# Kernel optimization log

Measured on AMD Instinct MI355X. Metric: run time of the kernel, lower is better.

Reference implementation:

```python
import jax, jax.numpy as jnp
import numpy as np

TOTAL_LABELS = 21
TOTAL_POS = 128
TOTAL_NEG = 128
VARIANCES = jnp.asarray([0.1, 0.1, 0.2, 0.2], dtype=jnp.float32)


def _make_boxes(key, shape):
    # valid [y1,x1,y2,x2] boxes with y2>y1, x2>x1 in [0,1]
    k1, k2 = jax.random.split(key)
    lo = jax.random.uniform(k1, shape + (2,), dtype=jnp.float32) * 0.6
    sz = jax.random.uniform(k2, shape + (2,), dtype=jnp.float32) * 0.4 + 1e-3
    return jnp.concatenate([lo, lo + sz], axis=-1)


def setup_inputs() -> dict:
    key = jax.random.key(0)
    kr, kg, kl, kp, kn = jax.random.split(key, 5)
    B, N, M = 64, 3000, 128
    roi_bboxes = _make_boxes(kr, (B, N))
    gt_boxes = _make_boxes(kg, (B, M))
    gt_labels = jax.random.randint(kl, (B, M), 1, TOTAL_LABELS).astype(jnp.int32)
    maxval = max(TOTAL_POS, TOTAL_NEG) * 10  # matches tf.random.uniform(minval=1, maxval=10*count)
    rand_pos = jax.random.randint(kp, (B, N), 1, maxval).astype(jnp.int32)
    rand_neg = jax.random.randint(kn, (B, N), 1, maxval).astype(jnp.int32)
    return {"roi_bboxes": roi_bboxes, "gt_boxes": gt_boxes, "gt_labels": gt_labels,
            "rand_pos": rand_pos, "rand_neg": rand_neg}


def _iou_map(roi, gt):
    # roi: [B,N,4], gt: [B,M,4] -> iou: [B,N,M]
    r = roi[:, :, None, :]
    g = gt[:, None, :, :]
    iy1 = jnp.maximum(r[..., 0], g[..., 0])
    ix1 = jnp.maximum(r[..., 1], g[..., 1])
    iy2 = jnp.minimum(r[..., 2], g[..., 2])
    ix2 = jnp.minimum(r[..., 3], g[..., 3])
    inter = jnp.maximum(iy2 - iy1, 0.0) * jnp.maximum(ix2 - ix1, 0.0)
    area_r = (r[..., 2] - r[..., 0]) * (r[..., 3] - r[..., 1])
    area_g = (g[..., 2] - g[..., 0]) * (g[..., 3] - g[..., 1])
    return inter / (area_r + area_g - inter + 1e-7)


def _random_select(mask, rand_ints, count):
    # faithful port of train_utils.randomly_select_xyz_mask: rank by mask*rand, keep top `count`
    mult = mask.astype(jnp.int32) * rand_ints
    order = jnp.argsort(-mult, axis=-1)
    ranks = jnp.argsort(order, axis=-1)
    return mask & (ranks < count)


def _get_deltas(bboxes, gt):
    bw = bboxes[..., 3] - bboxes[..., 1]
    bh = bboxes[..., 2] - bboxes[..., 0]
    bcx = bboxes[..., 1] + 0.5 * bw
    bcy = bboxes[..., 0] + 0.5 * bh
    gw = gt[..., 3] - gt[..., 1]
    gh = gt[..., 2] - gt[..., 0]
    gcx = gt[..., 1] + 0.5 * gw
    gcy = gt[..., 0] + 0.5 * gh
    bw = jnp.where(bw == 0.0, 1e-3, bw)
    bh = jnp.where(bh == 0.0, 1e-3, bh)
    dx = jnp.where(gw == 0.0, 0.0, (gcx - bcx) / bw)
    dy = jnp.where(gh == 0.0, 0.0, (gcy - bcy) / bh)
    dw = jnp.where(gw == 0.0, 0.0, jnp.log(jnp.where(gw == 0.0, 1.0, gw / bw)))
    dh = jnp.where(gh == 0.0, 0.0, jnp.log(jnp.where(gh == 0.0, 1.0, gh / bh)))
    return jnp.stack([dy, dx, dh, dw], axis=-1)


def reference(roi_bboxes, gt_boxes, gt_labels, rand_pos, rand_neg):
    B, N = roi_bboxes.shape[:2]
    iou = _iou_map(roi_bboxes, gt_boxes)                      # [B,N,M]
    best_gt = jnp.argmax(iou, axis=2)                         # [B,N]
    best_iou = jnp.max(iou, axis=2)                           # [B,N]
    pos_mask = _random_select(best_iou > 0.5, rand_pos, TOTAL_POS)
    neg_mask = _random_select((best_iou < 0.5) & (best_iou > 0.1), rand_neg, TOTAL_NEG)
    gt_boxes_map = jnp.take_along_axis(gt_boxes, best_gt[:, :, None], axis=1)   # [B,N,4]
    expanded_gt_boxes = jnp.where(pos_mask[..., None], gt_boxes_map, 0.0)
    gt_labels_map = jnp.take_along_axis(gt_labels, best_gt, axis=1)             # [B,N]
    pos_gt_labels = jnp.where(pos_mask, gt_labels_map, -1)
    expanded_gt_labels = pos_gt_labels + neg_mask.astype(jnp.int32)
    deltas = _get_deltas(roi_bboxes, expanded_gt_boxes) / VARIANCES             # [B,N,4]
    roi_bbox_labels = jax.nn.one_hot(expanded_gt_labels, TOTAL_LABELS, dtype=deltas.dtype)  # [B,N,L]
    # broadcast-multiply scatter: place deltas into the slot of the assigned label
    roi_bbox_deltas = roi_bbox_labels[..., None] * deltas[:, :, None, :]        # [B,N,L,4]
    roi_bbox_deltas = roi_bbox_deltas.reshape(B, N * TOTAL_LABELS, 4)
    return (jax.lax.stop_gradient(roi_bbox_deltas), jax.lax.stop_gradient(roi_bbox_labels))
```

## Files before the change

### kernel.cpp

```cpp
#include <hip/hip_runtime.h>

#define BB 64
#define NN 3000
#define MM 128
#define NBINS 1280
#define NSEL 128

__global__ __launch_bounds__(256) void k1_iou(
    const float4* __restrict__ roi, const float4* __restrict__ gt,
    const int* __restrict__ gtl, const int* __restrict__ rpos,
    const int* __restrict__ rneg, int* __restrict__ packed,
    float4* __restrict__ deltas, float4* __restrict__ out1z)
{
  #pragma clang fp contract(off)
  const int b = blockIdx.y;
  const int n = blockIdx.x * 256 + threadIdx.x;
  const bool valid = (n < NN);
  __shared__ float4 g[MM];
  __shared__ float  ga[MM];
  __shared__ int    gl[MM];

  float4 r = roi[b * NN + (valid ? n : 0)];
  if (threadIdx.x < MM) {
    float4 v = gt[b * MM + threadIdx.x];
    g[threadIdx.x]  = v;
    ga[threadIdx.x] = (v.z - v.x) * (v.w - v.y);
    gl[threadIdx.x] = gtl[b * MM + threadIdx.x];
  }
  __syncthreads();

  {
    const float4 z = make_float4(0.f, 0.f, 0.f, 0.f);
    const int gid = (blockIdx.y * gridDim.x + blockIdx.x) * 256 + threadIdx.x;
    for (int i = gid; i < BB * NN * 21; i += 768 * 256) out1z[i] = z;
  }

  if (!valid) return;
  float ar = (r.z - r.x) * (r.w - r.y);
  float best = -1.0f; int bi = 0;
  #pragma unroll 4
  for (int m = 0; m < MM; ++m) {
    float4 gm = g[m];
    float iy1 = fmaxf(r.x, gm.x);
    float ix1 = fmaxf(r.y, gm.y);
    float iy2 = fminf(r.z, gm.z);
    float ix2 = fminf(r.w, gm.w);
    float inter = fmaxf(iy2 - iy1, 0.0f) * fmaxf(ix2 - ix1, 0.0f);
    float iou = inter / (ar + ga[m] - inter + 1e-7f);
    if (iou > best) { best = iou; bi = m; }
  }
  int pm = (best > 0.5f) ? rpos[b * NN + n] : 0;
  int nm = (best < 0.5f && best > 0.1f) ? rneg[b * NN + n] : 0;
  packed[b * NN + n] = pm | (nm << 11) | (gl[bi] << 22);

  float4 gg = g[bi];
  float bw = r.w - r.y, bh = r.z - r.x;
  float bcx = r.y + 0.5f * bw, bcy = r.x + 0.5f * bh;
  float gw = gg.w - gg.y, gh = gg.z - gg.x;
  float gcx = gg.y + 0.5f * gw, gcy = gg.x + 0.5f * gh;
  bw = (bw == 0.0f) ? 0.001f : bw;
  bh = (bh == 0.0f) ? 0.001f : bh;
  float dx = (gw == 0.0f) ? 0.0f : (gcx - bcx) / bw;
  float dy = (gh == 0.0f) ? 0.0f : (gcy - bcy) / bh;
  float dw = (gw == 0.0f) ? 0.0f : logf(gw / bw);
  float dh = (gh == 0.0f) ? 0.0f : logf(gh / bh);
  deltas[b * NN + n] = make_float4(dy / 0.1f, dx / 0.1f, dh / 0.2f, dw / 0.2f);
}

__global__ __launch_bounds__(1024) void k2_select(
    const int* __restrict__ packed, const float4* __restrict__ deltas,
    float4* __restrict__ out1, float* __restrict__ out2)
{
  const int b = blockIdx.x;
  const int tid = threadIdx.x;
  const int lane = tid & 63;
  const int wave = tid >> 6;
  __shared__ int sp[NN];
  __shared__ unsigned hist[NBINS + 1];
  __shared__ unsigned wsum[16];
  __shared__ int sT[4];

  for (int i = tid; i < NBINS + 1; i += 1024) hist[i] = 0;
  if (tid == 0) { sT[0] = 0; sT[1] = 0; sT[2] = 0; sT[3] = 0; }
  __syncthreads();

  for (int i = tid; i < NN; i += 1024) {
    int p = packed[b * NN + i];
    sp[i] = p;
    int pm = p & 0x7FF, nm = (p >> 11) & 0x7FF;
    if (pm) atomicAdd(&hist[pm], 1u);
    if (nm) atomicAdd(&hist[nm], 0x10000u);
  }
  __syncthreads();

  if (wave == 0) {
    unsigned cs[21];
    const int base = 1 + lane * 20;
    cs[20] = 0;
    #pragma unroll
    for (int j = 19; j >= 0; --j) cs[j] = cs[j + 1] + hist[base + j];
    unsigned tot = cs[0];
    unsigned run = tot;
    #pragma unroll
    for (int off = 1; off < 64; off <<= 1) {
      unsigned u = __shfl_down(run, off);
      if (lane + off < 64) run += u;
    }
    unsigned above = run - tot;
    #pragma unroll
    for (int j = 0; j < 20; ++j) {
      int bin = base + j;
      unsigned s  = cs[j] + above;
      unsigned sn = cs[j + 1] + above;
      unsigned ps = s & 0xFFFFu, psn = sn & 0xFFFFu;
      if (ps >= NSEL && psn < NSEL) { sT[0] = bin; sT[1] = NSEL - (int)psn; }
      unsigned ns = s >> 16, nsn = sn >> 16;
      if (ns >= NSEL && nsn < NSEL) { sT[2] = bin; sT[3] = NSEL - (int)nsn; }
    }
  }
  __syncthreads();
  const int Tp = sT[0], Qp = sT[1], Tn = sT[2], Qn = sT[3];

  const int n0 = tid * 3;
  int p0 = 0, p1 = 0, p2 = 0;
  if (n0     < NN) p0 = sp[n0];
  if (n0 + 1 < NN) p1 = sp[n0 + 1];
  if (n0 + 2 < NN) p2 = sp[n0 + 2];
  unsigned cc = 0;
  {
    int q[3] = {p0, p1, p2};
    #pragma unroll
    for (int j = 0; j < 3; ++j) {
      int pm = q[j] & 0x7FF, nm = (q[j] >> 11) & 0x7FF;
      if (Tp && pm == Tp) cc += 1u;
      if (Tn && nm == Tn) cc += 0x10000u;
    }
  }
  unsigned inc = cc;
  #pragma unroll
  for (int off = 1; off < 64; off <<= 1) {
    unsigned u = __shfl_up(inc, off);
    if (lane >= off) inc += u;
  }
  if (lane == 63) wsum[wave] = inc;
  __syncthreads();
  unsigned woff = 0;
  for (int w = 0; w < wave; ++w) woff += wsum[w];
  unsigned excl = woff + (inc - cc);
  int ep = (int)(excl & 0xFFFFu), en = (int)(excl >> 16);

  int q[3] = {p0, p1, p2};
  #pragma unroll
  for (int j = 0; j < 3; ++j) {
    int n = n0 + j;
    if (n >= NN) break;
    int p = q[j];
    int pm = p & 0x7FF, nm = (p >> 11) & 0x7FF;
    bool selp;
    if (pm > Tp) selp = true;
    else if (pm && pm == Tp) { selp = (ep < Qp); ep++; }
    else selp = false;
    bool seln;
    if (nm > Tn) seln = true;
    else if (nm && nm == Tn) { seln = (en < Qn); en++; }
    else seln = false;
    int lab = selp ? ((p >> 22) & 0x1F) : (seln ? 0 : -1);
    sp[n] = lab;
    if (lab > 0) {
      size_t nl = (size_t)b * NN + n;
      out1[nl * 21 + lab] = deltas[nl];
    }
  }
  __syncthreads();

  float* o2 = out2 + (size_t)b * NN * 21;
  for (int u = tid; u < NN * 21; u += 1024) {
    int n = u / 21;
    int c = u - n * 21;
    o2[u] = (c == sp[n]) ? 1.0f : 0.0f;
  }
}

extern "C" void kernel_launch(void* const* d_in, const int* in_sizes, int n_in,
                              void* d_out, int out_size, void* d_ws, size_t ws_size,
                              hipStream_t stream) {
  const float4* roi = (const float4*)d_in[0];
  const float4* gt  = (const float4*)d_in[1];
  const int* gtl  = (const int*)d_in[2];
  const int* rpos = (const int*)d_in[3];
  const int* rneg = (const int*)d_in[4];

  char* ws = (char*)d_ws;
  int*    packed = (int*)ws;
  float4* deltas = (float4*)(ws + (1 << 20));

  float4* out1 = (float4*)d_out;
  float*  out2 = (float*)d_out + (size_t)BB * NN * 21 * 4;

  dim3 g1((NN + 255) / 256, BB);
  k1_iou<<<g1, 256, 0, stream>>>(roi, gt, gtl, rpos, rneg, packed, deltas, out1);
  k2_select<<<BB, 1024, 0, stream>>>(packed, deltas, out1, out2);
}
```

Before: 48.08 us.

## Zero both outputs in a dedicated kernel and scatter one-hot labels sparsely

```diff
diff --git a/kernel.cpp b/kernel.cpp
--- a/kernel.cpp
+++ b/kernel.cpp
@@ -6,11 +6,17 @@
 #define NBINS 1280
 #define NSEL 128
 
+__global__ __launch_bounds__(256) void k0_zero(float4* __restrict__ o, int n4)
+{
+  int i = blockIdx.x * 256 + threadIdx.x;
+  if (i < n4) o[i] = make_float4(0.f, 0.f, 0.f, 0.f);
+}
+
 __global__ __launch_bounds__(256) void k1_iou(
     const float4* __restrict__ roi, const float4* __restrict__ gt,
     const int* __restrict__ gtl, const int* __restrict__ rpos,
     const int* __restrict__ rneg, int* __restrict__ packed,
-    float4* __restrict__ deltas, float4* __restrict__ out1z)
+    float4* __restrict__ deltas)
 {
   #pragma clang fp contract(off)
   const int b = blockIdx.y;
@@ -28,14 +34,8 @@
     gl[threadIdx.x] = gtl[b * MM + threadIdx.x];
   }
   __syncthreads();
+  if (!valid) return;
 
-  {
-    const float4 z = make_float4(0.f, 0.f, 0.f, 0.f);
-    const int gid = (blockIdx.y * gridDim.x + blockIdx.x) * 256 + threadIdx.x;
-    for (int i = gid; i < BB * NN * 21; i += 768 * 256) out1z[i] = z;
-  }
-
-  if (!valid) return;
   float ar = (r.z - r.x) * (r.w - r.y);
   float best = -1.0f; int bi = 0;
   #pragma unroll 4
@@ -122,19 +122,16 @@
   const int Tp = sT[0], Qp = sT[1], Tn = sT[2], Qn = sT[3];
 
   const int n0 = tid * 3;
-  int p0 = 0, p1 = 0, p2 = 0;
-  if (n0     < NN) p0 = sp[n0];
-  if (n0 + 1 < NN) p1 = sp[n0 + 1];
-  if (n0 + 2 < NN) p2 = sp[n0 + 2];
+  int q[3] = {0, 0, 0};
+  if (n0     < NN) q[0] = sp[n0];
+  if (n0 + 1 < NN) q[1] = sp[n0 + 1];
+  if (n0 + 2 < NN) q[2] = sp[n0 + 2];
   unsigned cc = 0;
-  {
-    int q[3] = {p0, p1, p2};
-    #pragma unroll
-    for (int j = 0; j < 3; ++j) {
-      int pm = q[j] & 0x7FF, nm = (q[j] >> 11) & 0x7FF;
-      if (Tp && pm == Tp) cc += 1u;
-      if (Tn && nm == Tn) cc += 0x10000u;
-    }
+  #pragma unroll
+  for (int j = 0; j < 3; ++j) {
+    int pm = q[j] & 0x7FF, nm = (q[j] >> 11) & 0x7FF;
+    if (Tp && pm == Tp) cc += 1u;
+    if (Tn && nm == Tn) cc += 0x10000u;
   }
   unsigned inc = cc;
   #pragma unroll
@@ -149,7 +146,6 @@
   unsigned excl = woff + (inc - cc);
   int ep = (int)(excl & 0xFFFFu), en = (int)(excl >> 16);
 
-  int q[3] = {p0, p1, p2};
   #pragma unroll
   for (int j = 0; j < 3; ++j) {
     int n = n0 + j;
@@ -164,20 +160,12 @@
     if (nm > Tn) seln = true;
     else if (nm && nm == Tn) { seln = (en < Qn); en++; }
     else seln = false;
-    int lab = selp ? ((p >> 22) & 0x1F) : (seln ? 0 : -1);
-    sp[n] = lab;
-    if (lab > 0) {
+    if (selp | seln) {
       size_t nl = (size_t)b * NN + n;
-      out1[nl * 21 + lab] = deltas[nl];
+      int lab = selp ? ((p >> 22) & 0x1F) : 0;
+      out2[nl * 21 + lab] = 1.0f;
+      if (lab > 0) out1[nl * 21 + lab] = deltas[nl];
     }
-  }
-  __syncthreads();
-
-  float* o2 = out2 + (size_t)b * NN * 21;
-  for (int u = tid; u < NN * 21; u += 1024) {
-    int n = u / 21;
-    int c = u - n * 21;
-    o2[u] = (c == sp[n]) ? 1.0f : 0.0f;
   }
 }
 
@@ -197,7 +185,9 @@
   float4* out1 = (float4*)d_out;
   float*  out2 = (float*)d_out + (size_t)BB * NN * 21 * 4;
 
+  const int n4 = (BB * NN * 21 * 5) / 4;
+  k0_zero<<<(n4 + 255) / 256, 256, 0, stream>>>((float4*)d_out, n4);
   dim3 g1((NN + 255) / 256, BB);
-  k1_iou<<<g1, 256, 0, stream>>>(roi, gt, gtl, rpos, rneg, packed, deltas, out1);
+  k1_iou<<<g1, 256, 0, stream>>>(roi, gt, gtl, rpos, rneg, packed, deltas);
   k2_select<<<BB, 1024, 0, stream>>>(packed, deltas, out1, out2);
 }
```

After: 47.45 us. Within noise of the previous version (-1.3%).
